# Kernel optimization log

Hardware: AMD Instinct MI355X
Metric: run time of the kernel (lower is better)

## Reference

```python
import jax, jax.numpy as jnp
import numpy as np

NUM_BLOCKS_PER_ROW = 64
NUM_BLOCKS_PER_COLUMN = 36
N = NUM_BLOCKS_PER_ROW * NUM_BLOCKS_PER_COLUMN  # 2304 nodes per frame
F = 32   # frames in the GOP (linear reference chain)
B = 1024  # batch = number of candidate anchor points
S = 256   # selected anchor points


def setup_inputs() -> dict:
    key = jax.random.key(0)
    k1, k2, k3, k4 = jax.random.split(key, 4)
    # weights[f] propagates cumulated error from frame f -> frame f+1; scaled small
    # so the 31-step propagation chain stays numerically tame.
    weights = jax.random.normal(k1, (F - 1, N, N), dtype=jnp.float32) * 0.02
    biases = jax.random.uniform(k2, (F, N), dtype=jnp.float32)  # per-frame tc bias
    selected_anchor_points = jax.random.randint(k3, (S, 3), 0, 32, dtype=jnp.int32)
    candidate_anchor_points = jax.random.randint(k4, (B, 3), 0, 32, dtype=jnp.int32)
    return {
        "weights": weights,
        "biases": biases,
        "selected_anchor_points": selected_anchor_points,
        "candidate_anchor_points": candidate_anchor_points,
    }


def _forward(weights, biases, selected_anchor_points, candidate_anchor_points):
    dtype = biases.dtype
    # flatten (row, col) -> node index, same as row * num_blocks_per_row + col
    sel_f = selected_anchor_points[:, 0]
    sel_node = selected_anchor_points[:, 1] * NUM_BLOCKS_PER_ROW + selected_anchor_points[:, 2]
    cand_f = candidate_anchor_points[:, 0]
    cand_node = candidate_anchor_points[:, 1] * NUM_BLOCKS_PER_ROW + candidate_anchor_points[:, 2]

    # selected anchors zero a node's column for ALL batch rows in their frame
    keep_sel = jnp.ones((F, N), dtype=dtype).at[sel_f, sel_node].set(0.0)  # [F, N]
    # candidate anchors zero one (batch, node) entry in their frame
    cand_oh = jax.nn.one_hot(cand_node, N, dtype=dtype)  # [B, N]

    def apply_masks(err, f):
        # err: [B, N] cumulated error of frame f
        err = err * keep_sel[f][None, :]
        kill = (cand_f == f).astype(dtype)[:, None] * cand_oh  # [B, N]
        return err * (1.0 - kill)

    # root (key) frame: bias only
    err0 = apply_masks(jnp.broadcast_to(biases[0], (B, N)), 0)
    total0 = jnp.sum(err0, axis=1)  # [B]

    def step(carry, xs):
        prev_err, total = carry
        w_f, b_f, f = xs
        # torch.sparse.mm(W, prev.T).T == prev @ W.T
        cur = b_f[None, :] + jnp.matmul(prev_err, w_f.T)  # [B, N]
        cur = apply_masks(cur, f)
        return (cur, total + jnp.sum(cur, axis=1)), None

    frame_ids = jnp.arange(1, F)
    (_, total), _ = jax.lax.scan(step, (err0, total0), (weights, biases[1:], frame_ids))
    return total  # [B] per-candidate summed error


def reference(weights, biases, selected_anchor_points, candidate_anchor_points):
    return _forward(weights, biases, selected_anchor_points, candidate_anchor_points)
```

## Files before the change

kernel.cpp:

```cpp
#include <hip/hip_runtime.h>
#include <stdint.h>

#define NN 2304
#define NF 32
#define NB 1024
#define NS 256

#define BM 128
#define BN 96
#define BK 64
#define KSLICES (NN / BK)
#define DEPTH 4

typedef short bf16x8 __attribute__((ext_vector_type(8)));
typedef float f32x4  __attribute__((ext_vector_type(4)));

__device__ __forceinline__ unsigned short f2bf(float f) {
  union { float f; unsigned u; } v; v.f = f;
  return (unsigned short)((v.u + 0x7FFFu + ((v.u >> 16) & 1u)) >> 16);
}

__device__ __forceinline__ void async16(const void* g, void* l) {
  __builtin_amdgcn_global_load_lds((const __attribute__((address_space(1))) void*)g,
                                   (__attribute__((address_space(3))) void*)l, 16, 0, 0);
}

__global__ void init_kernel(const f32x4* __restrict__ W4, const int* __restrict__ sel,
                            const int* __restrict__ cand, bf16x8* __restrict__ Wb8,
                            float* __restrict__ keep, int* __restrict__ cf,
                            int* __restrict__ cn) {
  int gid = blockIdx.x * 256 + threadIdx.x;
  if (gid < (31 * NN * NN) / 8) {
    f32x4 x = W4[2 * gid], y = W4[2 * gid + 1];
    bf16x8 o;
    o[0] = (short)f2bf(x[0]); o[1] = (short)f2bf(x[1]);
    o[2] = (short)f2bf(x[2]); o[3] = (short)f2bf(x[3]);
    o[4] = (short)f2bf(y[0]); o[5] = (short)f2bf(y[1]);
    o[6] = (short)f2bf(y[2]); o[7] = (short)f2bf(y[3]);
    Wb8[gid] = o;
  }
  if (gid < NF * NN) {
    int f = gid / NN, n = gid - f * NN;
    float v = 1.0f;
    for (int s = 0; s < NS; ++s) {
      int sf = sel[3 * s], sn = sel[3 * s + 1] * 64 + sel[3 * s + 2];
      if (sf == f && sn == n) v = 0.0f;
    }
    keep[gid] = v;
  }
  if (gid < NB) {
    cf[gid] = cand[3 * gid];
    cn[gid] = cand[3 * gid + 1] * 64 + cand[3 * gid + 2];
  }
}

__global__ void frame0_kernel(const float* __restrict__ bias0, const float* __restrict__ keep0,
                              const int* __restrict__ cf, const int* __restrict__ cn,
                              unsigned short* __restrict__ err, float* __restrict__ out) {
  int b = blockIdx.x, t = threadIdx.x;
  int kn = (cf[b] == 0) ? cn[b] : -1;
  float sum = 0.f;
  for (int j = t; j < NN; j += 256) {
    float v = bias0[j] * keep0[j];
    if (j == kn) v = 0.f;
    err[b * NN + j] = f2bf(v);
    sum += v;
  }
  for (int m = 32; m; m >>= 1) sum += __shfl_down(sum, m, 64);
  __shared__ float red[4];
  if ((t & 63) == 0) red[t >> 6] = sum;
  __syncthreads();
  if (t == 0) out[b] = red[0] + red[1] + red[2] + red[3];
}

#define WAITV(n) asm volatile("s_waitcnt vmcnt(" #n ")" ::: "memory")

__launch_bounds__(512, 2)
__global__ void gemm_frame(const unsigned short* __restrict__ Ain,
                           const unsigned short* __restrict__ Wf,
                           const float* __restrict__ biasf,
                           const float* __restrict__ keepf,
                           const int* __restrict__ cf, const int* __restrict__ cn,
                           int f, unsigned short* __restrict__ errOut,
                           float* __restrict__ out) {
  __shared__ __align__(16) unsigned char sA[DEPTH][BM * BK * 2];
  __shared__ __align__(16) unsigned char sB[DEPTH][BN * BK * 2];

  const int t = threadIdx.x;
  const int l = t & 63, w = t >> 6;
  const int wm = w >> 1, wn = w & 1;

  const int id = blockIdx.x;
  const int swz = (id & 7) * 24 + (id >> 3);
  const int mBase = (swz / 24) * BM;
  const int nBase = (swz % 24) * BN;

  const int sRow = l >> 3;
  const int sCk = (l & 7) ^ sRow;
  const bool aRole = (w < 4);
  const int rw = aRole ? w : (w - 4);
  const unsigned short* gSrc = aRole
      ? Ain + (mBase + rw * 32 + sRow) * NN + sCk * 8
      : Wf  + (nBase + rw * 24 + sRow) * NN + sCk * 8;

  auto issue = [&](int s, int buf) {
    const unsigned short* g = gSrc + s * BK;
    if (aRole) {
      unsigned char* la = &sA[buf][rw * 32 * 128 + l * 16];
#pragma unroll
      for (int c = 0; c < 4; ++c) async16(g + c * 8 * NN, la + c * 8 * 128);
    } else {
      unsigned char* lb = &sB[buf][rw * 24 * 128 + l * 16];
#pragma unroll
      for (int c = 0; c < 3; ++c) async16(g + c * 8 * NN, lb + c * 8 * 128);
    }
  };

  const int fl = l & 15, q = l >> 4;
  const int fragB0 = (q ^ (fl & 7)) * 16;

  f32x4 acc[2][3];
#pragma unroll
  for (int r = 0; r < 2; ++r)
#pragma unroll
    for (int c = 0; c < 3; ++c) acc[r][c] = (f32x4){0.f, 0.f, 0.f, 0.f};

  issue(0, 0); issue(1, 1); issue(2, 2); issue(3, 3);

  int buf = 0;
  for (int s = 0; s < KSLICES; ++s) {
    const int ahead = KSLICES - 1 - s;
    if (ahead >= 3) { if (aRole) WAITV(12); else WAITV(9); }
    else if (ahead == 2) { if (aRole) WAITV(8); else WAITV(6); }
    else if (ahead == 1) { if (aRole) WAITV(4); else WAITV(3); }
    else { WAITV(0); }
    asm volatile("s_barrier" ::: "memory");

    const unsigned char* pa = &sA[buf][(wm * 32 + fl) * 128];
    const unsigned char* pb = &sB[buf][(wn * 48 + fl) * 128];
#pragma unroll
    for (int h = 0; h < 2; ++h) {
      const int cb = fragB0 ^ (h * 64);
      bf16x8 aF[2], bF[3];
#pragma unroll
      for (int r = 0; r < 2; ++r) aF[r] = *(const bf16x8*)(pa + r * 2048 + cb);
#pragma unroll
      for (int c = 0; c < 3; ++c) bF[c] = *(const bf16x8*)(pb + c * 2048 + cb);
#pragma unroll
      for (int r = 0; r < 2; ++r)
#pragma unroll
        for (int c = 0; c < 3; ++c)
          acc[r][c] = __builtin_amdgcn_mfma_f32_16x16x32_bf16(aF[r], bF[c], acc[r][c], 0, 0, 0);
    }
    asm volatile("s_waitcnt lgkmcnt(0)\n\ts_barrier" ::: "memory");
    if (s + DEPTH < KSLICES) issue(s + DEPTH, buf);
    buf = (buf == DEPTH - 1) ? 0 : buf + 1;
  }

#pragma unroll
  for (int r = 0; r < 2; ++r) {
    float rs[4] = {0.f, 0.f, 0.f, 0.f};
    const int rowB = mBase + wm * 32 + r * 16 + q * 4;
#pragma unroll
    for (int c = 0; c < 3; ++c) {
      const int col = nBase + wn * 48 + c * 16 + fl;
      const float kv = keepf[col], bv = biasf[col];
#pragma unroll
      for (int i = 0; i < 4; ++i) {
        const int row = rowB + i;
        float v = (acc[r][c][i] + bv) * kv;
        if (cf[row] == f && cn[row] == col) v = 0.f;
        errOut[row * NN + col] = f2bf(v);
        rs[i] += v;
      }
    }
#pragma unroll
    for (int m = 1; m < 16; m <<= 1) {
#pragma unroll
      for (int i = 0; i < 4; ++i) rs[i] += __shfl_xor(rs[i], m, 64);
    }
    if (fl == 0) {
#pragma unroll
      for (int i = 0; i < 4; ++i) atomicAdd(&out[rowB + i], rs[i]);
    }
  }
}

extern "C" void kernel_launch(void* const* d_in, const int* in_sizes, int n_in,
                              void* d_out, int out_size, void* d_ws, size_t ws_size,
                              hipStream_t stream) {
  (void)in_sizes; (void)n_in; (void)out_size; (void)ws_size;
  const float* W = (const float*)d_in[0];
  const float* biases = (const float*)d_in[1];
  const int* sel = (const int*)d_in[2];
  const int* cand = (const int*)d_in[3];
  float* out = (float*)d_out;
  char* ws = (char*)d_ws;

  size_t off = 0;
  unsigned short* Wb = (unsigned short*)(ws + off); off += (size_t)31 * NN * NN * 2;
  float* keep = (float*)(ws + off); off += (size_t)NF * NN * 4;
  int* cf = (int*)(ws + off); off += NB * 4;
  int* cn = (int*)(ws + off); off += NB * 4;
  off = (off + 255) & ~(size_t)255;
  unsigned short* errA = (unsigned short*)(ws + off); off += (size_t)NB * NN * 2;
  unsigned short* errB = (unsigned short*)(ws + off);

  int convBlocks = (31 * NN * NN / 8 + 255) / 256;
  init_kernel<<<convBlocks, 256, 0, stream>>>((const f32x4*)W, sel, cand, (bf16x8*)Wb,
                                              keep, cf, cn);
  frame0_kernel<<<NB, 256, 0, stream>>>(biases, keep, cf, cn, errA, out);
  for (int f = 1; f < NF; ++f) {
    const unsigned short* Ain = (f & 1) ? errA : errB;
    unsigned short* Aout = (f & 1) ? errB : errA;
    gemm_frame<<<(NN / BN) * (NB / BM), 512, 0, stream>>>(
        Ain, Wb + (size_t)(f - 1) * NN * NN, biases + f * NN, keep + f * NN,
        cf, cn, f, Aout, out);
  }
}
```

Measured before the change: 2.237 ms.

## Fuse per-frame GEMM launches into one persistent cooperative kernel with group barriers

Replaces the 31 per-frame GEMM launches and the frame-0 kernel with one persistent cooperative kernel. Each group of 24 blocks owning the same 128 batch rows synchronises between frames via an atomic counter barrier, since rows only depend on themselves across frames. This removes kernel launch gaps and tail effects between frames, but adds spin-wait barriers and lets groups fall out of step, which can change L2 reuse of weight tiles. Output zeroing and barrier counters are initialised in the conversion kernel.

```diff
diff --git a/kernel.cpp b/kernel.cpp
--- a/kernel.cpp
+++ b/kernel.cpp
@@ -11,6 +11,8 @@
 #define BK 64
 #define KSLICES (NN / BK)
 #define DEPTH 4
+#define NGRP 8
+#define GRPBLKS 24
 
 typedef short bf16x8 __attribute__((ext_vector_type(8)));
 typedef float f32x4  __attribute__((ext_vector_type(4)));
@@ -25,10 +27,13 @@
                                    (__attribute__((address_space(3))) void*)l, 16, 0, 0);
 }
 
+#define WAITV(n) asm volatile("s_waitcnt vmcnt(" #n ")" ::: "memory")
+
 __global__ void init_kernel(const f32x4* __restrict__ W4, const int* __restrict__ sel,
                             const int* __restrict__ cand, bf16x8* __restrict__ Wb8,
                             float* __restrict__ keep, int* __restrict__ cf,
-                            int* __restrict__ cn) {
+                            int* __restrict__ cn, float* __restrict__ out,
+                            int* __restrict__ bar) {
   int gid = blockIdx.x * 256 + threadIdx.x;
   if (gid < (31 * NN * NN) / 8) {
     f32x4 x = W4[2 * gid], y = W4[2 * gid + 1];
@@ -51,138 +56,169 @@
   if (gid < NB) {
     cf[gid] = cand[3 * gid];
     cn[gid] = cand[3 * gid + 1] * 64 + cand[3 * gid + 2];
-  }
-}
-
-__global__ void frame0_kernel(const float* __restrict__ bias0, const float* __restrict__ keep0,
-                              const int* __restrict__ cf, const int* __restrict__ cn,
-                              unsigned short* __restrict__ err, float* __restrict__ out) {
-  int b = blockIdx.x, t = threadIdx.x;
-  int kn = (cf[b] == 0) ? cn[b] : -1;
-  float sum = 0.f;
-  for (int j = t; j < NN; j += 256) {
-    float v = bias0[j] * keep0[j];
-    if (j == kn) v = 0.f;
-    err[b * NN + j] = f2bf(v);
-    sum += v;
-  }
-  for (int m = 32; m; m >>= 1) sum += __shfl_down(sum, m, 64);
-  __shared__ float red[4];
-  if ((t & 63) == 0) red[t >> 6] = sum;
+    out[gid] = 0.f;
+  }
+  if (gid < NGRP * NF) bar[gid] = 0;
+}
+
+__device__ __forceinline__ void group_barrier(int* cnt, int t) {
   __syncthreads();
-  if (t == 0) out[b] = red[0] + red[1] + red[2] + red[3];
-}
-
-#define WAITV(n) asm volatile("s_waitcnt vmcnt(" #n ")" ::: "memory")
+  if (t == 0) {
+    __builtin_amdgcn_fence(__ATOMIC_RELEASE, "agent");
+    __hip_atomic_fetch_add(cnt, 1, __ATOMIC_RELAXED, __HIP_MEMORY_SCOPE_AGENT);
+    while (__hip_atomic_load(cnt, __ATOMIC_RELAXED, __HIP_MEMORY_SCOPE_AGENT) < GRPBLKS)
+      __builtin_amdgcn_s_sleep(2);
+    __builtin_amdgcn_fence(__ATOMIC_ACQUIRE, "agent");
+  }
+  __syncthreads();
+}
 
 __launch_bounds__(512, 2)
-__global__ void gemm_frame(const unsigned short* __restrict__ Ain,
-                           const unsigned short* __restrict__ Wf,
-                           const float* __restrict__ biasf,
-                           const float* __restrict__ keepf,
-                           const int* __restrict__ cf, const int* __restrict__ cn,
-                           int f, unsigned short* __restrict__ errOut,
-                           float* __restrict__ out) {
+__global__ void persist_kernel(const unsigned short* __restrict__ Wb,
+                               const float* __restrict__ biases,
+                               const float* __restrict__ keep,
+                               const int* __restrict__ cf, const int* __restrict__ cn,
+                               unsigned short* __restrict__ errA,
+                               unsigned short* __restrict__ errB,
+                               float* __restrict__ out, int* __restrict__ bar) {
   __shared__ __align__(16) unsigned char sA[DEPTH][BM * BK * 2];
   __shared__ __align__(16) unsigned char sB[DEPTH][BN * BK * 2];
 
   const int t = threadIdx.x;
   const int l = t & 63, w = t >> 6;
   const int wm = w >> 1, wn = w & 1;
-
   const int id = blockIdx.x;
-  const int swz = (id & 7) * 24 + (id >> 3);
-  const int mBase = (swz / 24) * BM;
-  const int nBase = (swz % 24) * BN;
+  const int g = id & 7;
+  const int mBase = g * BM;
+  const int nBase = (id >> 3) * BN;
+
+  {
+    const int row = mBase + (t >> 2);
+    const int c0 = nBase + (t & 3) * 24;
+    const int kn = (cf[row] == 0) ? cn[row] : -1;
+    float sum = 0.f;
+    for (int j = 0; j < 24; ++j) {
+      const int col = c0 + j;
+      float v = biases[col] * keep[col];
+      if (col == kn) v = 0.f;
+      errA[row * NN + col] = f2bf(v);
+      sum += v;
+    }
+    sum += __shfl_xor(sum, 1, 64);
+    sum += __shfl_xor(sum, 2, 64);
+    if ((t & 3) == 0) atomicAdd(&out[row], sum);
+  }
+  group_barrier(&bar[g * NF + 0], t);
 
   const int sRow = l >> 3;
   const int sCk = (l & 7) ^ sRow;
   const bool aRole = (w < 4);
   const int rw = aRole ? w : (w - 4);
-  const unsigned short* gSrc = aRole
-      ? Ain + (mBase + rw * 32 + sRow) * NN + sCk * 8
-      : Wf  + (nBase + rw * 24 + sRow) * NN + sCk * 8;
-
-  auto issue = [&](int s, int buf) {
-    const unsigned short* g = gSrc + s * BK;
-    if (aRole) {
-      unsigned char* la = &sA[buf][rw * 32 * 128 + l * 16];
-#pragma unroll
-      for (int c = 0; c < 4; ++c) async16(g + c * 8 * NN, la + c * 8 * 128);
-    } else {
-      unsigned char* lb = &sB[buf][rw * 24 * 128 + l * 16];
-#pragma unroll
-      for (int c = 0; c < 3; ++c) async16(g + c * 8 * NN, lb + c * 8 * 128);
-    }
-  };
+  const int ldsOff = aRole ? (rw * 32 * 128 + l * 16) : (rw * 24 * 128 + l * 16);
+  const int gRowOff = aRole ? ((mBase + rw * 32 + sRow) * NN + sCk * 8)
+                            : ((nBase + rw * 24 + sRow) * NN + sCk * 8);
 
   const int fl = l & 15, q = l >> 4;
   const int fragB0 = (q ^ (fl & 7)) * 16;
 
-  f32x4 acc[2][3];
-#pragma unroll
-  for (int r = 0; r < 2; ++r)
-#pragma unroll
-    for (int c = 0; c < 3; ++c) acc[r][c] = (f32x4){0.f, 0.f, 0.f, 0.f};
-
-  issue(0, 0); issue(1, 1); issue(2, 2); issue(3, 3);
-
-  int buf = 0;
-  for (int s = 0; s < KSLICES; ++s) {
-    const int ahead = KSLICES - 1 - s;
-    if (ahead >= 3) { if (aRole) WAITV(12); else WAITV(9); }
-    else if (ahead == 2) { if (aRole) WAITV(8); else WAITV(6); }
-    else if (ahead == 1) { if (aRole) WAITV(4); else WAITV(3); }
-    else { WAITV(0); }
-    asm volatile("s_barrier" ::: "memory");
-
-    const unsigned char* pa = &sA[buf][(wm * 32 + fl) * 128];
-    const unsigned char* pb = &sB[buf][(wn * 48 + fl) * 128];
-#pragma unroll
-    for (int h = 0; h < 2; ++h) {
-      const int cb = fragB0 ^ (h * 64);
-      bf16x8 aF[2], bF[3];
-#pragma unroll
-      for (int r = 0; r < 2; ++r) aF[r] = *(const bf16x8*)(pa + r * 2048 + cb);
-#pragma unroll
-      for (int c = 0; c < 3; ++c) bF[c] = *(const bf16x8*)(pb + c * 2048 + cb);
-#pragma unroll
-      for (int r = 0; r < 2; ++r)
-#pragma unroll
-        for (int c = 0; c < 3; ++c)
-          acc[r][c] = __builtin_amdgcn_mfma_f32_16x16x32_bf16(aF[r], bF[c], acc[r][c], 0, 0, 0);
-    }
-    asm volatile("s_waitcnt lgkmcnt(0)\n\ts_barrier" ::: "memory");
-    if (s + DEPTH < KSLICES) issue(s + DEPTH, buf);
-    buf = (buf == DEPTH - 1) ? 0 : buf + 1;
-  }
-
-#pragma unroll
-  for (int r = 0; r < 2; ++r) {
-    float rs[4] = {0.f, 0.f, 0.f, 0.f};
-    const int rowB = mBase + wm * 32 + r * 16 + q * 4;
-#pragma unroll
-    for (int c = 0; c < 3; ++c) {
-      const int col = nBase + wn * 48 + c * 16 + fl;
-      const float kv = keepf[col], bv = biasf[col];
-#pragma unroll
-      for (int i = 0; i < 4; ++i) {
-        const int row = rowB + i;
-        float v = (acc[r][c][i] + bv) * kv;
-        if (cf[row] == f && cn[row] == col) v = 0.f;
-        errOut[row * NN + col] = f2bf(v);
-        rs[i] += v;
-      }
-    }
-#pragma unroll
-    for (int m = 1; m < 16; m <<= 1) {
-#pragma unroll
-      for (int i = 0; i < 4; ++i) rs[i] += __shfl_xor(rs[i], m, 64);
-    }
-    if (fl == 0) {
-#pragma unroll
-      for (int i = 0; i < 4; ++i) atomicAdd(&out[rowB + i], rs[i]);
-    }
+  for (int f = 1; f < NF; ++f) {
+    const unsigned short* Ain = (f & 1) ? errA : errB;
+    unsigned short* errOut = (f & 1) ? errB : errA;
+    const unsigned short* gSrc =
+        (aRole ? Ain : Wb + (size_t)(f - 1) * NN * NN) + gRowOff;
+    const float* biasf = biases + f * NN;
+    const float* keepf = keep + f * NN;
+
+    f32x4 acc[2][3];
+#pragma unroll
+    for (int r = 0; r < 2; ++r)
+#pragma unroll
+      for (int c = 0; c < 3; ++c) acc[r][c] = (f32x4){0.f, 0.f, 0.f, 0.f};
+
+#pragma unroll
+    for (int p = 0; p < DEPTH; ++p) {
+      const unsigned short* gp = gSrc + p * BK;
+      if (aRole) {
+        unsigned char* la = &sA[p][ldsOff];
+#pragma unroll
+        for (int c = 0; c < 4; ++c) async16(gp + c * 8 * NN, la + c * 8 * 128);
+      } else {
+        unsigned char* lb = &sB[p][ldsOff];
+#pragma unroll
+        for (int c = 0; c < 3; ++c) async16(gp + c * 8 * NN, lb + c * 8 * 128);
+      }
+    }
+
+    int buf = 0;
+    for (int s = 0; s < KSLICES; ++s) {
+      const int ahead = KSLICES - 1 - s;
+      if (ahead >= 3) { if (aRole) WAITV(12); else WAITV(9); }
+      else if (ahead == 2) { if (aRole) WAITV(8); else WAITV(6); }
+      else if (ahead == 1) { if (aRole) WAITV(4); else WAITV(3); }
+      else { WAITV(0); }
+      asm volatile("s_barrier" ::: "memory");
+
+      const unsigned char* pa = &sA[buf][(wm * 32 + fl) * 128];
+      const unsigned char* pb = &sB[buf][(wn * 48 + fl) * 128];
+#pragma unroll
+      for (int h = 0; h < 2; ++h) {
+        const int cb = fragB0 ^ (h * 64);
+        bf16x8 aF[2], bF[3];
+#pragma unroll
+        for (int r = 0; r < 2; ++r) aF[r] = *(const bf16x8*)(pa + r * 2048 + cb);
+#pragma unroll
+        for (int c = 0; c < 3; ++c) bF[c] = *(const bf16x8*)(pb + c * 2048 + cb);
+#pragma unroll
+        for (int r = 0; r < 2; ++r)
+#pragma unroll
+          for (int c = 0; c < 3; ++c)
+            acc[r][c] = __builtin_amdgcn_mfma_f32_16x16x32_bf16(aF[r], bF[c], acc[r][c], 0, 0, 0);
+      }
+      asm volatile("s_waitcnt lgkmcnt(0)\n\ts_barrier" ::: "memory");
+      if (s + DEPTH < KSLICES) {
+        const unsigned short* gp = gSrc + (s + DEPTH) * BK;
+        if (aRole) {
+          unsigned char* la = &sA[buf][ldsOff];
+#pragma unroll
+          for (int c = 0; c < 4; ++c) async16(gp + c * 8 * NN, la + c * 8 * 128);
+        } else {
+          unsigned char* lb = &sB[buf][ldsOff];
+#pragma unroll
+          for (int c = 0; c < 3; ++c) async16(gp + c * 8 * NN, lb + c * 8 * 128);
+        }
+      }
+      buf = (buf == DEPTH - 1) ? 0 : buf + 1;
+    }
+
+#pragma unroll
+    for (int r = 0; r < 2; ++r) {
+      float rs[4] = {0.f, 0.f, 0.f, 0.f};
+      const int rowB = mBase + wm * 32 + r * 16 + q * 4;
+#pragma unroll
+      for (int c = 0; c < 3; ++c) {
+        const int col = nBase + wn * 48 + c * 16 + fl;
+        const float kv = keepf[col], bv = biasf[col];
+#pragma unroll
+        for (int i = 0; i < 4; ++i) {
+          const int row = rowB + i;
+          float v = (acc[r][c][i] + bv) * kv;
+          if (cf[row] == f && cn[row] == col) v = 0.f;
+          errOut[row * NN + col] = f2bf(v);
+          rs[i] += v;
+        }
+      }
+#pragma unroll
+      for (int m = 1; m < 16; m <<= 1) {
+#pragma unroll
+        for (int i = 0; i < 4; ++i) rs[i] += __shfl_xor(rs[i], m, 64);
+      }
+      if (fl == 0) {
+#pragma unroll
+        for (int i = 0; i < 4; ++i) atomicAdd(&out[rowB + i], rs[i]);
+      }
+    }
+
+    group_barrier(&bar[g * NF + f], t);
   }
 }
 
@@ -202,19 +238,23 @@
   float* keep = (float*)(ws + off); off += (size_t)NF * NN * 4;
   int* cf = (int*)(ws + off); off += NB * 4;
   int* cn = (int*)(ws + off); off += NB * 4;
+  int* bar = (int*)(ws + off); off += NGRP * NF * 4;
   off = (off + 255) & ~(size_t)255;
   unsigned short* errA = (unsigned short*)(ws + off); off += (size_t)NB * NN * 2;
   unsigned short* errB = (unsigned short*)(ws + off);
 
   int convBlocks = (31 * NN * NN / 8 + 255) / 256;
   init_kernel<<<convBlocks, 256, 0, stream>>>((const f32x4*)W, sel, cand, (bf16x8*)Wb,
-                                              keep, cf, cn);
-  frame0_kernel<<<NB, 256, 0, stream>>>(biases, keep, cf, cn, errA, out);
-  for (int f = 1; f < NF; ++f) {
-    const unsigned short* Ain = (f & 1) ? errA : errB;
-    unsigned short* Aout = (f & 1) ? errB : errA;
-    gemm_frame<<<(NN / BN) * (NB / BM), 512, 0, stream>>>(
-        Ain, Wb + (size_t)(f - 1) * NN * NN, biases + f * NN, keep + f * NN,
-        cf, cn, f, Aout, out);
-  }
-}
+                                              keep, cf, cn, out, bar);
+
+  const unsigned short* WbC = Wb;
+  void* kargs[] = {(void*)&WbC, (void*)&biases, (void*)&keep, (void*)&cf, (void*)&cn,
+                   (void*)&errA, (void*)&errB, (void*)&out, (void*)&bar};
+  hipError_t e = hipLaunchCooperativeKernel(
+      reinterpret_cast<void*>(persist_kernel), dim3(NGRP * GRPBLKS), dim3(512),
+      kargs, 0, stream);
+  if (e != hipSuccess) {
+    persist_kernel<<<NGRP * GRPBLKS, 512, 0, stream>>>(Wb, biases, keep, cf, cn,
+                                                       errA, errB, out, bar);
+  }
+}
```

After: 1.969 ms. 1.14x faster.
